# Kernel optimization log

Hardware: AMD Instinct MI355X
Metric: run time of the kernel (lower is better)

## Reference

```python
import jax, jax.numpy as jnp
import numpy as np

MARGIN = 0.1
PD_EPS = 1e-6  # torch.nn.PairwiseDistance default eps (added to the difference)

B = 4096
D = 512


def setup_inputs() -> dict:
    key = jax.random.key(0)
    k1, k2, k3 = jax.random.split(key, 3)
    return {
        "feature_ts": jax.random.normal(k1, (B, D), dtype=jnp.float32),
        "feature_image1": jax.random.normal(k2, (B, D), dtype=jnp.float32),
        "feature_image2": jax.random.normal(k3, (B, D), dtype=jnp.float32),
    }


def _safe_sqrt(sq):
    # sqrt with zero gradient at 0 (matches torch.cdist backward at zero distance)
    pos = sq > 0
    return jnp.where(pos, jnp.sqrt(jnp.where(pos, sq, 1.0)), 0.0)


def reference(feature_ts, feature_image1, feature_image2):
    b, d = feature_ts.shape
    # representations: [3B, D]
    reps = jnp.concatenate([feature_ts, feature_image1, feature_image2], axis=0)

    # cdist(feature_ts, reps, p=2) -> [B, 3B] via Gram-matrix expansion
    sq = (
        jnp.sum(feature_ts * feature_ts, axis=1)[:, None]
        + jnp.sum(reps * reps, axis=1)[None, :]
        - 2.0 * (feature_ts @ reps.T)
    )
    dist = _safe_sqrt(jnp.maximum(sq, 0.0))          # [B, 3B]
    dist = jax.nn.relu(dist)                          # faithful (no-op: dist >= 0)

    # PairwiseDistance(p=2): ||x1 - x2 + eps||_2
    diff = feature_image1 - feature_image2 + PD_EPS
    dist12 = jnp.sqrt(jnp.sum(diff * diff, axis=1))   # [B]

    idx = jnp.arange(b)
    l_pos_1 = dist[idx, idx + b]                      # diag offset B
    l_pos_2 = dist[idx, idx + 2 * b]                  # diag offset 2B

    positives = l_pos_1 + l_pos_2 + dist12            # [B]
    positive_value = jnp.maximum(l_pos_1, l_pos_2)    # [B]

    # negatives: all columns except {i, i+B, i+2B}; masked min instead of gather
    cols = jnp.arange(3 * b)[None, :]
    rows = idx[:, None]
    same = (cols == rows) | (cols == rows + b) | (cols == rows + 2 * b)
    negative_value = jnp.min(jnp.where(same, jnp.inf, dist), axis=1)  # [B]

    triplet = jax.nn.relu(positives - negative_value + MARGIN) + positive_value
    return jnp.sum(triplet) / b
```

## Files before the change

kernel.cpp:

```cpp
#include <hip/hip_runtime.h>
#include <hip/hip_bf16.h>

typedef unsigned short u16;
typedef unsigned int u32;
typedef __attribute__((ext_vector_type(8))) short bf16x8;
typedef __attribute__((ext_vector_type(4))) float f32x4;

#define NB 4096
#define ND 512
#define NREPS (3*NB)
#define BM 128
#define BN 256
#define BK 64
#define NKT (ND/BK)
#define ASZ (BM*BK)
#define BSZ (BN*BK)

#define GLD16(gp, lp)                                                         \
  __builtin_amdgcn_global_load_lds(                                           \
      (const __attribute__((address_space(1))) void*)(gp),                    \
      (__attribute__((address_space(3))) void*)(lp), 16, 0, 0)

__device__ __forceinline__ u16 f2bf(float f) {
  union { float f; u32 u; } v; v.f = f;
  u32 u = v.u;
  u32 r = (u + 0x7FFFu + ((u >> 16) & 1u)) >> 16;
  return (u16)r;
}

__global__ __launch_bounds__(256) void prep_all(
    const float* __restrict__ ts, const float* __restrict__ i1,
    const float* __restrict__ i2, u16* __restrict__ reps,
    float* __restrict__ norms, float* __restrict__ dist12,
    u32* __restrict__ minsq)
{
  const int r = blockIdx.x;
  const int tid = threadIdx.x;
  const int wave = tid >> 6, lane = tid & 63;

  if (wave < 3) {
    const float* src = (wave == 0) ? ts + (size_t)r * ND
                     : (wave == 1) ? i1 + (size_t)r * ND
                     :               i2 + (size_t)r * ND;
    const float4* s4 = (const float4*)src;
    float4 a = s4[lane*2+0];
    float4 b = s4[lane*2+1];
    float ss = a.x*a.x + a.y*a.y + a.z*a.z + a.w*a.w
             + b.x*b.x + b.y*b.y + b.z*b.z + b.w*b.w;
    uint4 pk;
    pk.x = (u32)f2bf(a.x) | ((u32)f2bf(a.y) << 16);
    pk.y = (u32)f2bf(a.z) | ((u32)f2bf(a.w) << 16);
    pk.z = (u32)f2bf(b.x) | ((u32)f2bf(b.y) << 16);
    pk.w = (u32)f2bf(b.z) | ((u32)f2bf(b.w) << 16);
    *(uint4*)(reps + (size_t)(wave*NB + r) * ND + lane*8) = pk;
    #pragma unroll
    for (int off = 32; off; off >>= 1) ss += __shfl_down(ss, off);
    if (lane == 0) norms[wave*NB + r] = ss;
  } else {
    const float4* a4 = (const float4*)(i1 + (size_t)r * ND);
    const float4* b4 = (const float4*)(i2 + (size_t)r * ND);
    float ss = 0.f;
    #pragma unroll
    for (int i = 0; i < 2; ++i) {
      float4 a = a4[lane*2+i], b = b4[lane*2+i];
      float d0 = a.x - b.x + 1e-6f, d1 = a.y - b.y + 1e-6f;
      float d2 = a.z - b.z + 1e-6f, d3 = a.w - b.w + 1e-6f;
      ss += d0*d0 + d1*d1 + d2*d2 + d3*d3;
    }
    #pragma unroll
    for (int off = 32; off; off >>= 1) ss += __shfl_down(ss, off);
    if (lane == 0) { dist12[r] = sqrtf(ss); minsq[r] = 0x7F800000u; }
  }
}

__global__ __launch_bounds__(512) void gemm_min(
    const u16* __restrict__ reps, const float* __restrict__ norms,
    u32* __restrict__ minsq, float* __restrict__ lpos1,
    float* __restrict__ lpos2)
{
  const int mx = blockIdx.x, ny = blockIdx.y;
  const int rowBase = mx * BM;
  const int colBase = ny * BN;
  const bool tsTile = (colBase < NB);
  if (tsTile && 2*ny > mx) return;

  __shared__ u16 As[ASZ];
  __shared__ u16 Bs[BSZ];
  const int tid  = threadIdx.x;
  const int lane = tid & 63;
  const int wave = tid >> 6;
  const int wr = wave >> 2;
  const int wc = wave & 3;
  const int fr = lane & 15, fg = lane >> 4;

  const int rloc = lane >> 3;
  const int sp   = lane & 7;
  const u16* srcA[2]; u16* dstA[2];
  const u16* srcB[4]; u16* dstB[4];
  #pragma unroll
  for (int i = 0; i < 2; ++i) {
    const int r = wave*16 + i*8 + rloc;
    const int g = sp ^ (r & 7);
    srcA[i] = reps + (size_t)(rowBase + r) * ND + g*8;
    dstA[i] = &As[(wave*16 + i*8) * BK];
  }
  #pragma unroll
  for (int i = 0; i < 4; ++i) {
    const int r = wave*32 + i*8 + rloc;
    const int g = sp ^ (r & 7);
    srcB[i] = reps + (size_t)(colBase + r) * ND + g*8;
    dstB[i] = &Bs[(wave*32 + i*8) * BK];
  }

  f32x4 acc[4][4];
  const f32x4 zero = {0.f, 0.f, 0.f, 0.f};
  #pragma unroll
  for (int i = 0; i < 4; ++i)
    #pragma unroll
    for (int j = 0; j < 4; ++j)
      acc[i][j] = zero;

  for (int kt = 0; kt < NKT; ++kt) {
    const int koff = kt * BK;
    #pragma unroll
    for (int i = 0; i < 2; ++i) GLD16(srcA[i] + koff, dstA[i]);
    #pragma unroll
    for (int i = 0; i < 4; ++i) GLD16(srcB[i] + koff, dstB[i]);
    __syncthreads();

    bf16x8 af[4][2], bfr[4][2];
    #pragma unroll
    for (int mf = 0; mf < 4; ++mf)
      #pragma unroll
      for (int ks = 0; ks < 2; ++ks) {
        const int rowA = wr*64 + mf*16 + fr;
        const int slot = ks*4 + fg;
        af[mf][ks]  = *(const bf16x8*)&As[rowA*BK + (slot ^ (rowA & 7))*8];
        const int rowB = wc*64 + mf*16 + fr;
        bfr[mf][ks] = *(const bf16x8*)&Bs[rowB*BK + (slot ^ (rowB & 7))*8];
      }
    #pragma unroll
    for (int ks = 0; ks < 2; ++ks)
      #pragma unroll
      for (int mf = 0; mf < 4; ++mf)
        #pragma unroll
        for (int nf = 0; nf < 4; ++nf)
          acc[mf][nf] = __builtin_amdgcn_mfma_f32_16x16x32_bf16(
              af[mf][ks], bfr[nf][ks], acc[mf][nf], 0, 0, 0);
    __syncthreads();
  }

  float ncol[4];
  #pragma unroll
  for (int nf = 0; nf < 4; ++nf)
    ncol[nf] = norms[colBase + wc*64 + nf*16 + fr];
  const float INF = __builtin_inff();
  float cmin[4] = {INF, INF, INF, INF};

  #pragma unroll
  for (int mf = 0; mf < 4; ++mf) {
    #pragma unroll
    for (int q = 0; q < 4; ++q) {
      const int r_g = rowBase + wr*64 + mf*16 + fg*4 + q;
      const float ntr = norms[r_g];
      float vm = INF;
      #pragma unroll
      for (int nf = 0; nf < 4; ++nf) {
        const int c_g = colBase + wc*64 + nf*16 + fr;
        const float dot = acc[mf][nf][q];
        const float sq = ntr + ncol[nf] - 2.0f * dot;
        if (c_g == r_g + NB)   lpos1[r_g] = sq;
        if (c_g == r_g + 2*NB) lpos2[r_g] = sq;
        const bool excl = (c_g == r_g) || (c_g == r_g + NB) || (c_g == r_g + 2*NB);
        const float v = excl ? INF : fmaxf(sq, 0.0f);
        vm = fminf(vm, v);
        cmin[nf] = fminf(cmin[nf], v);
      }
      #pragma unroll
      for (int off = 1; off < 16; off <<= 1)
        vm = fminf(vm, __shfl_xor(vm, off));
      if (fr == 0)
        atomicMin(minsq + r_g, __float_as_uint(vm));
    }
  }

  if (tsTile) {
    #pragma unroll
    for (int nf = 0; nf < 4; ++nf) {
      float cm = cmin[nf];
      cm = fminf(cm, __shfl_xor(cm, 16));
      cm = fminf(cm, __shfl_xor(cm, 32));
      if (fg == 0) {
        const int c_g = colBase + wc*64 + nf*16 + fr;
        atomicMin(minsq + c_g, __float_as_uint(cm));
      }
    }
  }
}

__global__ __launch_bounds__(1024) void finalize(
    const float* __restrict__ lpos1, const float* __restrict__ lpos2,
    const float* __restrict__ dist12, const u32* __restrict__ minsq,
    float* __restrict__ out)
{
  __shared__ float red[16];
  const int tid = threadIdx.x;
  float s = 0.f;
  for (int r = tid; r < NB; r += 1024) {
    float l1 = sqrtf(fmaxf(lpos1[r], 0.f));
    float l2 = sqrtf(fmaxf(lpos2[r], 0.f));
    float neg = sqrtf(__uint_as_float(minsq[r]));
    float pos = l1 + l2 + dist12[r];
    s += fmaxf(pos - neg + 0.1f, 0.f) + fmaxf(l1, l2);
  }
  #pragma unroll
  for (int off = 32; off; off >>= 1) s += __shfl_down(s, off);
  if ((tid & 63) == 0) red[tid >> 6] = s;
  __syncthreads();
  if (tid == 0) {
    float t = 0.f;
    #pragma unroll
    for (int i = 0; i < 16; ++i) t += red[i];
    out[0] = t * (1.0f / NB);
  }
}

extern "C" void kernel_launch(void* const* d_in, const int* in_sizes, int n_in,
                              void* d_out, int out_size, void* d_ws, size_t ws_size,
                              hipStream_t stream) {
  const float* ts = (const float*)d_in[0];
  const float* i1 = (const float*)d_in[1];
  const float* i2 = (const float*)d_in[2];
  float* out = (float*)d_out;

  char* p = (char*)d_ws;
  u16* reps    = (u16*)p;            p += (size_t)NREPS * ND * sizeof(u16);
  float* norms = (float*)p;          p += (size_t)NREPS * sizeof(float);
  float* dist12 = (float*)p;         p += (size_t)NB * sizeof(float);
  u32* minsq   = (u32*)p;            p += (size_t)NB * sizeof(u32);
  float* lpos1 = (float*)p;          p += (size_t)NB * sizeof(float);
  float* lpos2 = (float*)p;          p += (size_t)NB * sizeof(float);

  prep_all<<<NB, 256, 0, stream>>>(ts, i1, i2, reps, norms, dist12, minsq);
  dim3 grid(NB / BM, NREPS / BN);
  gemm_min<<<grid, 512, 0, stream>>>(reps, norms, minsq, lpos1, lpos2);
  finalize<<<1, 1024, 0, stream>>>(lpos1, lpos2, dist12, minsq, out);
}
```

Baseline: 150.7 us.

## Quantize representations to fp8 e4m3 and use fp8 MFMA for Gram GEMM

Converts the concatenated representations to fp8 e4m3 instead of bf16, doubles BK to 128 with a matching swizzled LDS layout, and uses the fp8 16x16x32 MFMA. This halves the intermediate storage and the global/LDS traffic and raises matrix throughput. The finalize reduction is spread over 16 blocks with an atomicAdd into an output zeroed in prep. The risk is reduced accuracy of distances and of the min-negative selection.

```diff
diff --git a/kernel.cpp b/kernel.cpp
--- a/kernel.cpp
+++ b/kernel.cpp
@@ -1,9 +1,10 @@
 #include <hip/hip_runtime.h>
 #include <hip/hip_bf16.h>
-
-typedef unsigned short u16;
+#include <hip/hip_fp8.h>
+
+typedef unsigned char u8;
 typedef unsigned int u32;
-typedef __attribute__((ext_vector_type(8))) short bf16x8;
+typedef long long i64;
 typedef __attribute__((ext_vector_type(4))) float f32x4;
 
 #define NB 4096
@@ -11,7 +12,7 @@
 #define NREPS (3*NB)
 #define BM 128
 #define BN 256
-#define BK 64
+#define BK 128
 #define NKT (ND/BK)
 #define ASZ (BM*BK)
 #define BSZ (BN*BK)
@@ -21,22 +22,21 @@
       (const __attribute__((address_space(1))) void*)(gp),                    \
       (__attribute__((address_space(3))) void*)(lp), 16, 0, 0)
 
-__device__ __forceinline__ u16 f2bf(float f) {
-  union { float f; u32 u; } v; v.f = f;
-  u32 u = v.u;
-  u32 r = (u + 0x7FFFu + ((u >> 16) & 1u)) >> 16;
-  return (u16)r;
+__device__ __forceinline__ u32 pk4(float a, float b, float c, float d) {
+  __hip_fp8_e4m3 qa(a), qb(b), qc(c), qd(d);
+  return (u32)qa.__x | ((u32)qb.__x << 8) | ((u32)qc.__x << 16) | ((u32)qd.__x << 24);
 }
 
 __global__ __launch_bounds__(256) void prep_all(
     const float* __restrict__ ts, const float* __restrict__ i1,
-    const float* __restrict__ i2, u16* __restrict__ reps,
+    const float* __restrict__ i2, u8* __restrict__ reps,
     float* __restrict__ norms, float* __restrict__ dist12,
-    u32* __restrict__ minsq)
+    u32* __restrict__ minsq, float* __restrict__ out)
 {
   const int r = blockIdx.x;
   const int tid = threadIdx.x;
   const int wave = tid >> 6, lane = tid & 63;
+  if (r == 0 && tid == 0) out[0] = 0.f;
 
   if (wave < 3) {
     const float* src = (wave == 0) ? ts + (size_t)r * ND
@@ -47,12 +47,10 @@
     float4 b = s4[lane*2+1];
     float ss = a.x*a.x + a.y*a.y + a.z*a.z + a.w*a.w
              + b.x*b.x + b.y*b.y + b.z*b.z + b.w*b.w;
-    uint4 pk;
-    pk.x = (u32)f2bf(a.x) | ((u32)f2bf(a.y) << 16);
-    pk.y = (u32)f2bf(a.z) | ((u32)f2bf(a.w) << 16);
-    pk.z = (u32)f2bf(b.x) | ((u32)f2bf(b.y) << 16);
-    pk.w = (u32)f2bf(b.z) | ((u32)f2bf(b.w) << 16);
-    *(uint4*)(reps + (size_t)(wave*NB + r) * ND + lane*8) = pk;
+    uint2 pk;
+    pk.x = pk4(a.x, a.y, a.z, a.w);
+    pk.y = pk4(b.x, b.y, b.z, b.w);
+    *(uint2*)(reps + (size_t)(wave*NB + r) * ND + lane*8) = pk;
     #pragma unroll
     for (int off = 32; off; off >>= 1) ss += __shfl_down(ss, off);
     if (lane == 0) norms[wave*NB + r] = ss;
@@ -73,8 +71,16 @@
   }
 }
 
+__device__ __forceinline__ i64 rd8(const u8* __restrict__ S, int row,
+                                   int s, int f) {
+  const int q = (2*s + (f >> 1)) ^ (row & 7);
+  return *(const i64*)&S[row*BK + q*16 + (f & 1)*8];
+}
+
+#define MFMA16(a,b,c) __builtin_amdgcn_mfma_f32_16x16x32_fp8_fp8((a),(b),(c),0,0,0)
+
 __global__ __launch_bounds__(512) void gemm_min(
-    const u16* __restrict__ reps, const float* __restrict__ norms,
+    const u8* __restrict__ reps, const float* __restrict__ norms,
     u32* __restrict__ minsq, float* __restrict__ lpos1,
     float* __restrict__ lpos2)
 {
@@ -84,8 +90,8 @@
   const bool tsTile = (colBase < NB);
   if (tsTile && 2*ny > mx) return;
 
-  __shared__ u16 As[ASZ];
-  __shared__ u16 Bs[BSZ];
+  __shared__ u8 As[ASZ];
+  __shared__ u8 Bs[BSZ];
   const int tid  = threadIdx.x;
   const int lane = tid & 63;
   const int wave = tid >> 6;
@@ -95,20 +101,19 @@
 
   const int rloc = lane >> 3;
   const int sp   = lane & 7;
-  const u16* srcA[2]; u16* dstA[2];
-  const u16* srcB[4]; u16* dstB[4];
+  const int g    = sp ^ rloc;
+  const u8* srcA[2]; u8* dstA[2];
+  const u8* srcB[4]; u8* dstB[4];
   #pragma unroll
   for (int i = 0; i < 2; ++i) {
     const int r = wave*16 + i*8 + rloc;
-    const int g = sp ^ (r & 7);
-    srcA[i] = reps + (size_t)(rowBase + r) * ND + g*8;
+    srcA[i] = reps + (size_t)(rowBase + r) * ND + g*16;
     dstA[i] = &As[(wave*16 + i*8) * BK];
   }
   #pragma unroll
   for (int i = 0; i < 4; ++i) {
     const int r = wave*32 + i*8 + rloc;
-    const int g = sp ^ (r & 7);
-    srcB[i] = reps + (size_t)(colBase + r) * ND + g*8;
+    srcB[i] = reps + (size_t)(colBase + r) * ND + g*16;
     dstB[i] = &Bs[(wave*32 + i*8) * BK];
   }
 
@@ -128,25 +133,21 @@
     for (int i = 0; i < 4; ++i) GLD16(srcB[i] + koff, dstB[i]);
     __syncthreads();
 
-    bf16x8 af[4][2], bfr[4][2];
+    i64 af[4][4], bfr[4][4];
     #pragma unroll
     for (int mf = 0; mf < 4; ++mf)
       #pragma unroll
-      for (int ks = 0; ks < 2; ++ks) {
-        const int rowA = wr*64 + mf*16 + fr;
-        const int slot = ks*4 + fg;
-        af[mf][ks]  = *(const bf16x8*)&As[rowA*BK + (slot ^ (rowA & 7))*8];
-        const int rowB = wc*64 + mf*16 + fr;
-        bfr[mf][ks] = *(const bf16x8*)&Bs[rowB*BK + (slot ^ (rowB & 7))*8];
+      for (int s = 0; s < 4; ++s) {
+        af[mf][s]  = rd8(As, wr*64 + mf*16 + fr, s, fg);
+        bfr[mf][s] = rd8(Bs, wc*64 + mf*16 + fr, s, fg);
       }
     #pragma unroll
-    for (int ks = 0; ks < 2; ++ks)
+    for (int s = 0; s < 4; ++s)
       #pragma unroll
       for (int mf = 0; mf < 4; ++mf)
         #pragma unroll
         for (int nf = 0; nf < 4; ++nf)
-          acc[mf][nf] = __builtin_amdgcn_mfma_f32_16x16x32_bf16(
-              af[mf][ks], bfr[nf][ks], acc[mf][nf], 0, 0, 0);
+          acc[mf][nf] = MFMA16(af[mf][s], bfr[nf][s], acc[mf][nf]);
     __syncthreads();
   }
 
@@ -198,31 +199,25 @@
   }
 }
 
-__global__ __launch_bounds__(1024) void finalize(
+__global__ __launch_bounds__(256) void finalize(
     const float* __restrict__ lpos1, const float* __restrict__ lpos2,
     const float* __restrict__ dist12, const u32* __restrict__ minsq,
     float* __restrict__ out)
 {
-  __shared__ float red[16];
+  __shared__ float red[4];
   const int tid = threadIdx.x;
-  float s = 0.f;
-  for (int r = tid; r < NB; r += 1024) {
-    float l1 = sqrtf(fmaxf(lpos1[r], 0.f));
-    float l2 = sqrtf(fmaxf(lpos2[r], 0.f));
-    float neg = sqrtf(__uint_as_float(minsq[r]));
-    float pos = l1 + l2 + dist12[r];
-    s += fmaxf(pos - neg + 0.1f, 0.f) + fmaxf(l1, l2);
-  }
+  const int r = blockIdx.x * 256 + tid;
+  float l1 = sqrtf(fmaxf(lpos1[r], 0.f));
+  float l2 = sqrtf(fmaxf(lpos2[r], 0.f));
+  float neg = sqrtf(__uint_as_float(minsq[r]));
+  float pos = l1 + l2 + dist12[r];
+  float s = fmaxf(pos - neg + 0.1f, 0.f) + fmaxf(l1, l2);
   #pragma unroll
   for (int off = 32; off; off >>= 1) s += __shfl_down(s, off);
   if ((tid & 63) == 0) red[tid >> 6] = s;
   __syncthreads();
-  if (tid == 0) {
-    float t = 0.f;
-    #pragma unroll
-    for (int i = 0; i < 16; ++i) t += red[i];
-    out[0] = t * (1.0f / NB);
-  }
+  if (tid == 0)
+    atomicAdd(out, (red[0] + red[1] + red[2] + red[3]) * (1.0f / NB));
 }
 
 extern "C" void kernel_launch(void* const* d_in, const int* in_sizes, int n_in,
@@ -234,15 +229,15 @@
   float* out = (float*)d_out;
 
   char* p = (char*)d_ws;
-  u16* reps    = (u16*)p;            p += (size_t)NREPS * ND * sizeof(u16);
+  u8* reps     = (u8*)p;             p += (size_t)NREPS * ND * sizeof(u8);
   float* norms = (float*)p;          p += (size_t)NREPS * sizeof(float);
   float* dist12 = (float*)p;         p += (size_t)NB * sizeof(float);
   u32* minsq   = (u32*)p;            p += (size_t)NB * sizeof(u32);
   float* lpos1 = (float*)p;          p += (size_t)NB * sizeof(float);
   float* lpos2 = (float*)p;          p += (size_t)NB * sizeof(float);
 
-  prep_all<<<NB, 256, 0, stream>>>(ts, i1, i2, reps, norms, dist12, minsq);
+  prep_all<<<NB, 256, 0, stream>>>(ts, i1, i2, reps, norms, dist12, minsq, out);
   dim3 grid(NB / BM, NREPS / BN);
   gemm_min<<<grid, 512, 0, stream>>>(reps, norms, minsq, lpos1, lpos2);
-  finalize<<<1, 1024, 0, stream>>>(lpos1, lpos2, dist12, minsq, out);
-}
+  finalize<<<16, 256, 0, stream>>>(lpos1, lpos2, dist12, minsq, out);
+}
```

After: 134.9 us. 1.12x faster.
